# Optimization experiments

Measured on AMD Instinct MI355X. Metric: run time of the kernel, lower is better.

## Reference

```python
import jax, jax.numpy as jnp
import numpy as np

B, L, D, H, DH, M = 2, 2048, 512, 8, 2048, 128  # batch, seq, d_model, heads, d_hidden, max_rel_pos
HD = D // H
EPS = 1e-5


def _ln(x, w, b):
    mu = jnp.mean(x, axis=-1, keepdims=True)
    var = jnp.mean((x - mu) ** 2, axis=-1, keepdims=True)
    return (x - mu) * jax.lax.rsqrt(var + EPS) * w + b


def setup_inputs() -> dict:
    key = jax.random.key(0)
    ks = jax.random.split(key, 8)
    s = 0.02  # init std for weights
    return {
        "x": jax.random.normal(ks[0], (B, L, D), jnp.float32),
        "ln1_w": jnp.ones((D,), jnp.float32),
        "ln1_b": jnp.zeros((D,), jnp.float32),
        "qkv_w": jax.random.normal(ks[1], (D, 3 * D), jnp.float32) * s,
        "qkv_b": jnp.zeros((3 * D,), jnp.float32),
        "out_w": jax.random.normal(ks[2], (D, D), jnp.float32) * s,
        "out_b": jnp.zeros((D,), jnp.float32),
        "rel_bias": jax.random.normal(ks[3], (H, 2 * M - 1), jnp.float32) * s,
        "gamma1": 1e-4 * jnp.ones((D,), jnp.float32),
        "ln2_w": jnp.ones((D,), jnp.float32),
        "ln2_b": jnp.zeros((D,), jnp.float32),
        "ffn_in_w": jax.random.normal(ks[4], (D, 2 * DH), jnp.float32) * s,
        "ffn_in_b": jnp.zeros((2 * DH,), jnp.float32),
        "ffn_out_w": jax.random.normal(ks[5], (DH, D), jnp.float32) * s,
        "ffn_out_b": jnp.zeros((D,), jnp.float32),
        "gamma2": 1e-4 * jnp.ones((D,), jnp.float32),
    }


def _forward(x, ln1_w, ln1_b, qkv_w, qkv_b, out_w, out_b, rel_bias, gamma1,
             ln2_w, ln2_b, ffn_in_w, ffn_in_b, ffn_out_w, ffn_out_b, gamma2):
    b, l, d = x.shape
    # --- PreNorm attention with T5-style relative position bias ---
    h = _ln(x, ln1_w, ln1_b)
    qkv = h @ qkv_w + qkv_b                           # [B, L, 3D]
    q, k, v = jnp.split(qkv, 3, axis=-1)
    q = q.reshape(b, l, H, HD)
    k = k.reshape(b, l, H, HD)
    v = v.reshape(b, l, H, HD)
    scale = 1.0 / jnp.sqrt(jnp.asarray(HD, x.dtype))
    scores = jnp.einsum("bqhd,bkhd->bhqk", q, k) * scale   # [B, H, L, L]
    # relative position bias: clip(i - j) indexed into learned table
    ctx = jnp.arange(l)[:, None] - jnp.arange(l)[None, :]
    ctx = jnp.clip(ctx, -(M - 1), M - 1) + (M - 1)          # [L, L] in [0, 2M-2]
    rel = rel_bias[:, ctx]                                  # [H, L, L]
    scores = scores + rel[None]
    attn = jax.nn.softmax(scores, axis=-1)
    o = jnp.einsum("bhqk,bkhd->bqhd", attn, v).reshape(b, l, d)
    o = o @ out_w + out_b
    x = x + o * gamma1                                      # LayerScale residual
    # --- PreNorm GEGLU FFN ---
    h2 = _ln(x, ln2_w, ln2_b)
    ab = h2 @ ffn_in_w + ffn_in_b                           # [B, L, 2*DH]
    a, bgate = jnp.split(ab, 2, axis=-1)
    f = jax.nn.gelu(bgate, approximate=False) * a
    f = f @ ffn_out_w + ffn_out_b
    x = x + f * gamma2
    return x, attn


def reference(x, ln1_w, ln1_b, qkv_w, qkv_b, out_w, out_b, rel_bias, gamma1,
              ln2_w, ln2_b, ffn_in_w, ffn_in_b, ffn_out_w, ffn_out_b, gamma2):
    return _forward(x, ln1_w, ln1_b, qkv_w, qkv_b, out_w, out_b, rel_bias, gamma1,
                    ln2_w, ln2_b, ffn_in_w, ffn_in_b, ffn_out_w, ffn_out_b, gamma2)
```

## Files before the change

### kernel.cpp

```cpp
#include <hip/hip_runtime.h>
#include <math.h>

typedef __attribute__((ext_vector_type(4))) float f32x4;
typedef __attribute__((ext_vector_type(8))) short bf16x8;
typedef __attribute__((ext_vector_type(4))) short s16x4;

__device__ __forceinline__ unsigned short f2bf(float f) {
  union { float f; unsigned u; } v; v.f = f;
  return (unsigned short)((v.u + 0x7fffu + ((v.u >> 16) & 1u)) >> 16);
}

__global__ void ln_kernel(const float* __restrict__ in, const float* __restrict__ w,
                          const float* __restrict__ b, float* __restrict__ out) {
  __shared__ float sh[4];
  const int t = threadIdx.x;
  const float* p = in + (size_t)blockIdx.x * 512;
  float a0 = p[t], a1 = p[t + 256];
  float s = a0 + a1;
#pragma unroll
  for (int o = 32; o; o >>= 1) s += __shfl_down(s, o);
  if ((t & 63) == 0) sh[t >> 6] = s;
  __syncthreads();
  s = sh[0] + sh[1] + sh[2] + sh[3];
  float mu = s * (1.0f / 512.0f);
  float d0 = a0 - mu, d1 = a1 - mu;
  float q = d0 * d0 + d1 * d1;
  __syncthreads();
#pragma unroll
  for (int o = 32; o; o >>= 1) q += __shfl_down(q, o);
  if ((t & 63) == 0) sh[t >> 6] = q;
  __syncthreads();
  q = sh[0] + sh[1] + sh[2] + sh[3];
  float rstd = rsqrtf(q * (1.0f / 512.0f) + 1e-5f);
  float* po = out + (size_t)blockIdx.x * 512;
  po[t]       = d0 * rstd * w[t] + b[t];
  po[t + 256] = d1 * rstd * w[t + 256] + b[t + 256];
}

__global__ void transpose_w(const float* __restrict__ in, unsigned short* __restrict__ out,
                            int ldi, int ldo, long ibs, long obs) {
  __shared__ float tile[32][33];
  const float* ip = in + (long)blockIdx.z * ibs;
  unsigned short* op = out + (long)blockIdx.z * obs;
  const int tx = threadIdx.x & 31;
  const int ty = threadIdx.x >> 5;
  const int n0 = blockIdx.x * 32, k0 = blockIdx.y * 32;
#pragma unroll
  for (int i = 0; i < 4; ++i)
    tile[ty + i * 8][tx] = ip[(size_t)(k0 + ty + i * 8) * ldi + n0 + tx];
  __syncthreads();
#pragma unroll
  for (int i = 0; i < 4; ++i)
    op[(size_t)(n0 + ty + i * 8) * ldo + k0 + tx] = f2bf(tile[tx][ty + i * 8]);
}

template <int WM, int WN, int TM, int TN, int EPI>
__global__ __launch_bounds__(256) void gemm_kernel(
    const float* __restrict__ A, const unsigned short* __restrict__ Bt,
    float* __restrict__ C, int K, int lda, int ldb, int ldc,
    const float* __restrict__ bias, const float* __restrict__ resid,
    const float* __restrict__ gamma) {
  constexpr int BM = WM * TM * 16;
  constexpr int BN = WN * TN * 16;
  __shared__ short As[BM * 32];
  __shared__ short Bs[BN * 32];

  const int tid = threadIdx.x;
  const int m0 = blockIdx.y * BM, n0 = blockIdx.x * BN;
  const int w = tid >> 6, lane = tid & 63;
  const int wm = w / WN, wn = w % WN;
  const int lrow = lane & 15, lq = lane >> 4;

  f32x4 acc[TM][TN];
#pragma unroll
  for (int i = 0; i < TM; ++i)
#pragma unroll
    for (int j = 0; j < TN; ++j) acc[i][j] = (f32x4){0.f, 0.f, 0.f, 0.f};

  for (int k0 = 0; k0 < K; k0 += 32) {
    __syncthreads();
#pragma unroll
    for (int it = 0; it < (BM * 8) / 256; ++it) {
      int c = it * 256 + tid;
      int row = c >> 3, col = (c & 7) << 2;
      float4 v = *(const float4*)(A + (size_t)(m0 + row) * lda + k0 + col);
      s16x4 r = {(short)f2bf(v.x), (short)f2bf(v.y), (short)f2bf(v.z), (short)f2bf(v.w)};
      *(s16x4*)(As + row * 32 + col) = r;
    }
#pragma unroll
    for (int it = 0; it < (BN * 4) / 256; ++it) {
      int c = it * 256 + tid;
      int row = c >> 2, col = (c & 3) << 3;
      *(bf16x8*)(Bs + row * 32 + col) =
          *(const bf16x8*)(Bt + (size_t)(n0 + row) * ldb + k0 + col);
    }
    __syncthreads();

    bf16x8 af[TM], bf[TN];
#pragma unroll
    for (int mi = 0; mi < TM; ++mi)
      af[mi] = *(const bf16x8*)(As + (wm * TM * 16 + mi * 16 + lrow) * 32 + lq * 8);
#pragma unroll
    for (int nj = 0; nj < TN; ++nj)
      bf[nj] = *(const bf16x8*)(Bs + (wn * TN * 16 + nj * 16 + lrow) * 32 + lq * 8);
#pragma unroll
    for (int mi = 0; mi < TM; ++mi)
#pragma unroll
      for (int nj = 0; nj < TN; ++nj)
        acc[mi][nj] = __builtin_amdgcn_mfma_f32_16x16x32_bf16(af[mi], bf[nj], acc[mi][nj], 0, 0, 0);
  }

#pragma unroll
  for (int mi = 0; mi < TM; ++mi) {
#pragma unroll
    for (int nj = 0; nj < TN; ++nj) {
      int gm0 = m0 + wm * TM * 16 + mi * 16 + lq * 4;
      int gn = n0 + wn * TN * 16 + nj * 16 + lrow;
#pragma unroll
      for (int r = 0; r < 4; ++r) {
        int gm = gm0 + r;
        size_t idx = (size_t)gm * ldc + gn;
        float v = acc[mi][nj][r];
        if constexpr (EPI == 0) {
          C[idx] = v + bias[gn];
        } else {
          C[idx] = resid[idx] + (v + bias[gn]) * gamma[gn];
        }
      }
    }
  }
}

__global__ __launch_bounds__(256) void ffn1_gate_kernel(
    const float* __restrict__ A, const unsigned short* __restrict__ Bt,
    float* __restrict__ F, const float* __restrict__ bias) {
  __shared__ short As[128 * 32];
  __shared__ short Bs[64 * 32];
  __shared__ short Bs2[64 * 32];

  const int tid = threadIdx.x;
  const int n0 = blockIdx.x * 64, m0 = blockIdx.y * 128;
  const int w = tid >> 6, lane = tid & 63;
  const int wm = w >> 1, wn = w & 1;
  const int lrow = lane & 15, lq = lane >> 4;

  f32x4 acca[4][2], accb[4][2];
#pragma unroll
  for (int i = 0; i < 4; ++i)
#pragma unroll
    for (int j = 0; j < 2; ++j) {
      acca[i][j] = (f32x4){0.f, 0.f, 0.f, 0.f};
      accb[i][j] = (f32x4){0.f, 0.f, 0.f, 0.f};
    }

  for (int k0 = 0; k0 < 512; k0 += 32) {
    __syncthreads();
#pragma unroll
    for (int it = 0; it < 4; ++it) {
      int c = it * 256 + tid;
      int row = c >> 3, col = (c & 7) << 2;
      float4 v = *(const float4*)(A + (size_t)(m0 + row) * 512 + k0 + col);
      s16x4 r = {(short)f2bf(v.x), (short)f2bf(v.y), (short)f2bf(v.z), (short)f2bf(v.w)};
      *(s16x4*)(As + row * 32 + col) = r;
    }
    {
      int row = tid >> 2, col = (tid & 3) << 3;
      *(bf16x8*)(Bs + row * 32 + col) =
          *(const bf16x8*)(Bt + (size_t)(n0 + row) * 512 + k0 + col);
      *(bf16x8*)(Bs2 + row * 32 + col) =
          *(const bf16x8*)(Bt + (size_t)(2048 + n0 + row) * 512 + k0 + col);
    }
    __syncthreads();

    bf16x8 af[4], ba[2], bb[2];
#pragma unroll
    for (int mi = 0; mi < 4; ++mi)
      af[mi] = *(const bf16x8*)(As + (wm * 64 + mi * 16 + lrow) * 32 + lq * 8);
#pragma unroll
    for (int nj = 0; nj < 2; ++nj) {
      ba[nj] = *(const bf16x8*)(Bs + (wn * 32 + nj * 16 + lrow) * 32 + lq * 8);
      bb[nj] = *(const bf16x8*)(Bs2 + (wn * 32 + nj * 16 + lrow) * 32 + lq * 8);
    }
#pragma unroll
    for (int mi = 0; mi < 4; ++mi)
#pragma unroll
      for (int nj = 0; nj < 2; ++nj) {
        acca[mi][nj] = __builtin_amdgcn_mfma_f32_16x16x32_bf16(af[mi], ba[nj], acca[mi][nj], 0, 0, 0);
        accb[mi][nj] = __builtin_amdgcn_mfma_f32_16x16x32_bf16(af[mi], bb[nj], accb[mi][nj], 0, 0, 0);
      }
  }

#pragma unroll
  for (int mi = 0; mi < 4; ++mi)
#pragma unroll
    for (int nj = 0; nj < 2; ++nj) {
      int gm0 = m0 + wm * 64 + mi * 16 + lq * 4;
      int gn = n0 + wn * 32 + nj * 16 + lrow;
#pragma unroll
      for (int r = 0; r < 4; ++r) {
        float a = acca[mi][nj][r] + bias[gn];
        float bg = accb[mi][nj][r] + bias[2048 + gn];
        float g = 0.5f * bg * (1.0f + erff(bg * 0.70710678118654752f));
        F[(size_t)(gm0 + r) * 2048 + gn] = g * a;
      }
    }
}

__global__ __launch_bounds__(256) void attn_fused(
    const float* __restrict__ qkv, const unsigned short* __restrict__ vt,
    const float* __restrict__ rel, float* __restrict__ attn, float* __restrict__ o) {
  __shared__ short q_lds[2 * 64 * 32];
  __shared__ short k_lds[2 * 128 * 32];
  __shared__ short p_lds[4 * 64 * 32];
  __shared__ short v_lds[4 * 64 * 32];
  __shared__ float rsum[64];
  __shared__ float rinv[64];

  const int tid = threadIdx.x;
  const int m0 = blockIdx.x * 64;
  const int bh = blockIdx.y;
  const int b = bh >> 3, h = bh & 7;
  const float* qbase = qkv + (size_t)(b * 2048) * 1536 + h * 64;
  const float* kbase = qbase + 512;
  const unsigned short* vbase = vt + (size_t)bh * 64 * 2048;
  float* abase = attn + (size_t)bh * 2048 * 2048;
  const float* relh = rel + h * 255;

  const int w = tid >> 6, lane = tid & 63;
  const int wm = w >> 1, wn = w & 1;
  const int lrow = lane & 15, lq = lane >> 4;

#pragma unroll
  for (int it = 0; it < 4; ++it) {
    int idx = it * 256 + tid;
    int row = idx >> 4, c4 = (idx & 15) << 2;
    float4 v = *(const float4*)(qbase + (size_t)(m0 + row) * 1536 + c4);
    s16x4 r = {(short)f2bf(v.x), (short)f2bf(v.y), (short)f2bf(v.z), (short)f2bf(v.w)};
    *(s16x4*)(q_lds + (c4 >> 5) * 2048 + row * 32 + (c4 & 31)) = r;
  }
  if (tid < 64) rsum[tid] = 0.f;

  float psum[2][4] = {{0.f, 0.f, 0.f, 0.f}, {0.f, 0.f, 0.f, 0.f}};

  for (int t = 0; t < 16; ++t) {
    const int kt0 = t * 128;
    __syncthreads();
#pragma unroll
    for (int it = 0; it < 8; ++it) {
      int idx = it * 256 + tid;
      int row = idx >> 4, c4 = (idx & 15) << 2;
      float4 v = *(const float4*)(kbase + (size_t)(kt0 + row) * 1536 + c4);
      s16x4 r = {(short)f2bf(v.x), (short)f2bf(v.y), (short)f2bf(v.z), (short)f2bf(v.w)};
      *(s16x4*)(k_lds + (c4 >> 5) * 4096 + row * 32 + (c4 & 31)) = r;
    }
    __syncthreads();

    f32x4 acc[2][4];
#pragma unroll
    for (int mi = 0; mi < 2; ++mi)
#pragma unroll
      for (int nj = 0; nj < 4; ++nj) acc[mi][nj] = (f32x4){0.f, 0.f, 0.f, 0.f};
#pragma unroll
    for (int c = 0; c < 2; ++c) {
      bf16x8 af[2], bfv[4];
#pragma unroll
      for (int mi = 0; mi < 2; ++mi)
        af[mi] = *(const bf16x8*)(q_lds + c * 2048 + (wm * 32 + mi * 16 + lrow) * 32 + lq * 8);
#pragma unroll
      for (int nj = 0; nj < 4; ++nj)
        bfv[nj] = *(const bf16x8*)(k_lds + c * 4096 + (wn * 64 + nj * 16 + lrow) * 32 + lq * 8);
#pragma unroll
      for (int mi = 0; mi < 2; ++mi)
#pragma unroll
        for (int nj = 0; nj < 4; ++nj)
          acc[mi][nj] = __builtin_amdgcn_mfma_f32_16x16x32_bf16(af[mi], bfv[nj], acc[mi][nj], 0, 0, 0);
    }
#pragma unroll
    for (int mi = 0; mi < 2; ++mi)
#pragma unroll
      for (int nj = 0; nj < 4; ++nj) {
        int kl = wn * 64 + nj * 16 + lrow;
#pragma unroll
        for (int r = 0; r < 4; ++r) {
          int r_loc = wm * 32 + mi * 16 + lq * 4 + r;
          int d = (m0 + r_loc) - (kt0 + kl);
          d = d < -127 ? -127 : (d > 127 ? 127 : d);
          float s = acc[mi][nj][r] * 0.125f + relh[d + 127];
          psum[mi][r] += __expf(s);
        }
      }
  }
#pragma unroll
  for (int off = 1; off < 16; off <<= 1)
#pragma unroll
    for (int mi = 0; mi < 2; ++mi)
#pragma unroll
      for (int r = 0; r < 4; ++r) psum[mi][r] += __shfl_xor(psum[mi][r], off);
  if (lrow == 0) {
#pragma unroll
    for (int mi = 0; mi < 2; ++mi)
#pragma unroll
      for (int r = 0; r < 4; ++r)
        atomicAdd(&rsum[wm * 32 + mi * 16 + lq * 4 + r], psum[mi][r]);
  }
  __syncthreads();
  if (tid < 64) rinv[tid] = 1.0f / rsum[tid];
  __syncthreads();
  float rv[2][4];
#pragma unroll
  for (int mi = 0; mi < 2; ++mi)
#pragma unroll
    for (int r = 0; r < 4; ++r) rv[mi][r] = rinv[wm * 32 + mi * 16 + lq * 4 + r];

  f32x4 oacc[2][2];
#pragma unroll
  for (int mi = 0; mi < 2; ++mi)
#pragma unroll
    for (int nj = 0; nj < 2; ++nj) oacc[mi][nj] = (f32x4){0.f, 0.f, 0.f, 0.f};

  for (int t = 0; t < 16; ++t) {
    const int kt0 = t * 128;
    __syncthreads();
#pragma unroll
    for (int it = 0; it < 8; ++it) {
      int idx = it * 256 + tid;
      int row = idx >> 4, c4 = (idx & 15) << 2;
      float4 v = *(const float4*)(kbase + (size_t)(kt0 + row) * 1536 + c4);
      s16x4 r = {(short)f2bf(v.x), (short)f2bf(v.y), (short)f2bf(v.z), (short)f2bf(v.w)};
      *(s16x4*)(k_lds + (c4 >> 5) * 4096 + row * 32 + (c4 & 31)) = r;
    }
#pragma unroll
    for (int it = 0; it < 4; ++it) {
      int idx = it * 256 + tid;
      int dd = idx >> 4, c8 = (idx & 15) << 3;
      *(bf16x8*)(v_lds + (c8 >> 5) * 2048 + dd * 32 + (c8 & 31)) =
          *(const bf16x8*)(vbase + (size_t)dd * 2048 + kt0 + c8);
    }
    __syncthreads();

    f32x4 acc[2][4];
#pragma unroll
    for (int mi = 0; mi < 2; ++mi)
#pragma unroll
      for (int nj = 0; nj < 4; ++nj) acc[mi][nj] = (f32x4){0.f, 0.f, 0.f, 0.f};
#pragma unroll
    for (int c = 0; c < 2; ++c) {
      bf16x8 af[2], bfv[4];
#pragma unroll
      for (int mi = 0; mi < 2; ++mi)
        af[mi] = *(const bf16x8*)(q_lds + c * 2048 + (wm * 32 + mi * 16 + lrow) * 32 + lq * 8);
#pragma unroll
      for (int nj = 0; nj < 4; ++nj)
        bfv[nj] = *(const bf16x8*)(k_lds + c * 4096 + (wn * 64 + nj * 16 + lrow) * 32 + lq * 8);
#pragma unroll
      for (int mi = 0; mi < 2; ++mi)
#pragma unroll
        for (int nj = 0; nj < 4; ++nj)
          acc[mi][nj] = __builtin_amdgcn_mfma_f32_16x16x32_bf16(af[mi], bfv[nj], acc[mi][nj], 0, 0, 0);
    }
#pragma unroll
    for (int mi = 0; mi < 2; ++mi)
#pragma unroll
      for (int nj = 0; nj < 4; ++nj) {
        int kl = wn * 64 + nj * 16 + lrow;
#pragma unroll
        for (int r = 0; r < 4; ++r) {
          int r_loc = wm * 32 + mi * 16 + lq * 4 + r;
          int d = (m0 + r_loc) - (kt0 + kl);
          d = d < -127 ? -127 : (d > 127 ? 127 : d);
          float s = acc[mi][nj][r] * 0.125f + relh[d + 127];
          float e = __expf(s) * rv[mi][r];
          __builtin_nontemporal_store(e, abase + (size_t)(m0 + r_loc) * 2048 + kt0 + kl);
          p_lds[(kl >> 5) * 2048 + r_loc * 32 + (kl & 31)] = (short)f2bf(e);
        }
      }
    __syncthreads();

#pragma unroll
    for (int c2 = 0; c2 < 4; ++c2) {
      bf16x8 ap[2], bv[2];
#pragma unroll
      for (int mi = 0; mi < 2; ++mi)
        ap[mi] = *(const bf16x8*)(p_lds + c2 * 2048 + (wm * 32 + mi * 16 + lrow) * 32 + lq * 8);
#pragma unroll
      for (int nj = 0; nj < 2; ++nj)
        bv[nj] = *(const bf16x8*)(v_lds + c2 * 2048 + (wn * 32 + nj * 16 + lrow) * 32 + lq * 8);
#pragma unroll
      for (int mi = 0; mi < 2; ++mi)
#pragma unroll
        for (int nj = 0; nj < 2; ++nj)
          oacc[mi][nj] = __builtin_amdgcn_mfma_f32_16x16x32_bf16(ap[mi], bv[nj], oacc[mi][nj], 0, 0, 0);
    }
  }

#pragma unroll
  for (int mi = 0; mi < 2; ++mi)
#pragma unroll
    for (int nj = 0; nj < 2; ++nj) {
      int dd = wn * 32 + nj * 16 + lrow;
#pragma unroll
      for (int r = 0; r < 4; ++r) {
        int rr = m0 + wm * 32 + mi * 16 + lq * 4 + r;
        o[(size_t)(b * 2048 + rr) * 512 + h * 64 + dd] = oacc[mi][nj][r];
      }
    }
}

extern "C" void kernel_launch(void* const* d_in, const int* in_sizes, int n_in,
                              void* d_out, int out_size, void* d_ws, size_t ws_size,
                              hipStream_t stream) {
  (void)in_sizes; (void)n_in; (void)out_size; (void)ws_size;
  const float* x        = (const float*)d_in[0];
  const float* ln1_w    = (const float*)d_in[1];
  const float* ln1_b    = (const float*)d_in[2];
  const float* qkv_w    = (const float*)d_in[3];
  const float* qkv_b    = (const float*)d_in[4];
  const float* out_w    = (const float*)d_in[5];
  const float* out_b    = (const float*)d_in[6];
  const float* rel_bias = (const float*)d_in[7];
  const float* gamma1   = (const float*)d_in[8];
  const float* ln2_w    = (const float*)d_in[9];
  const float* ln2_b    = (const float*)d_in[10];
  const float* ffn_in_w = (const float*)d_in[11];
  const float* ffn_in_b = (const float*)d_in[12];
  const float* ffn_out_w  = (const float*)d_in[13];
  const float* ffn_out_b  = (const float*)d_in[14];
  const float* gamma2   = (const float*)d_in[15];

  float* x_out = (float*)d_out;
  float* attn  = x_out + (size_t)2 * 2048 * 512;

  float* ws  = (float*)d_ws;
  float* h   = ws;
  float* qkv = h + 2097152;
  float* o   = qkv + 6291456;
  float* x1  = o + 2097152;
  float* f   = x1 + 2097152;
  unsigned short* bt_qkv  = (unsigned short*)(f + 8388608);
  unsigned short* bt_out  = bt_qkv + 786432;
  unsigned short* bt_ffn1 = bt_out + 262144;
  unsigned short* bt_ffn2 = bt_ffn1 + 2097152;
  unsigned short* vt      = bt_ffn2 + 1048576;

  transpose_w<<<dim3(48, 16, 1), 256, 0, stream>>>(qkv_w,     bt_qkv,  1536, 512,  0, 0);
  transpose_w<<<dim3(16, 16, 1), 256, 0, stream>>>(out_w,     bt_out,  512,  512,  0, 0);
  transpose_w<<<dim3(128, 16, 1), 256, 0, stream>>>(ffn_in_w, bt_ffn1, 4096, 512,  0, 0);
  transpose_w<<<dim3(16, 64, 1), 256, 0, stream>>>(ffn_out_w, bt_ffn2, 512,  2048, 0, 0);

  ln_kernel<<<4096, 256, 0, stream>>>(x, ln1_w, ln1_b, h);

  gemm_kernel<2, 2, 4, 4, 0><<<dim3(12, 32, 1), 256, 0, stream>>>(
      h, bt_qkv, qkv, 512, 512, 512, 1536, qkv_b, nullptr, nullptr);

  transpose_w<<<dim3(2, 64, 8), 256, 0, stream>>>(
      qkv + 1024, vt, 1536, 2048, 64, (long)64 * 2048);
  transpose_w<<<dim3(2, 64, 8), 256, 0, stream>>>(
      qkv + (size_t)2048 * 1536 + 1024, vt + (size_t)8 * 64 * 2048, 1536, 2048, 64,
      (long)64 * 2048);

  attn_fused<<<dim3(32, 16, 1), 256, 0, stream>>>(qkv, vt, rel_bias, attn, o);

  gemm_kernel<2, 2, 4, 4, 3><<<dim3(4, 32, 1), 256, 0, stream>>>(
      o, bt_out, x1, 512, 512, 512, 512, out_b, x, gamma1);

  ln_kernel<<<4096, 256, 0, stream>>>(x1, ln2_w, ln2_b, h);

  ffn1_gate_kernel<<<dim3(32, 32, 1), 256, 0, stream>>>(h, bt_ffn1, f, ffn_in_b);

  gemm_kernel<2, 2, 4, 4, 3><<<dim3(4, 32, 1), 256, 0, stream>>>(
      f, bt_ffn2, x_out, 2048, 2048, 2048, 512, ffn_out_b, x1, gamma2);
}
```

Baseline: 641.6 us.

## Rework attention kernel to read bf16 operands directly and shrink tiles

The QKV GEMM now also writes a bf16 copy of its output, so the attention kernel loads Q/K fragments straight from global memory into registers and no longer converts and stages them in LDS. The attention tile shrinks to 32 query rows, with swizzled block ordering and a per-wave P buffer that uses an XOR swizzle. The relative-bias exponentials are precomputed once per block, and key tiles far from the diagonal take a constant-bias fast path. The GEMM tile sizes are also halved to launch more blocks. The exchange is more redundant global K/V reads per block and extra bf16 writes, in return for fewer block barriers and less LDS traffic.

```diff
diff --git a/kernel.cpp b/kernel.cpp
--- a/kernel.cpp
+++ b/kernel.cpp
@@ -57,7 +57,8 @@
 template <int WM, int WN, int TM, int TN, int EPI>
 __global__ __launch_bounds__(256) void gemm_kernel(
     const float* __restrict__ A, const unsigned short* __restrict__ Bt,
-    float* __restrict__ C, int K, int lda, int ldb, int ldc,
+    float* __restrict__ C, unsigned short* __restrict__ Cbf,
+    int K, int lda, int ldb, int ldc,
     const float* __restrict__ bias, const float* __restrict__ resid,
     const float* __restrict__ gamma) {
   constexpr int BM = WM * TM * 16;
@@ -123,6 +124,10 @@
         float v = acc[mi][nj][r];
         if constexpr (EPI == 0) {
           C[idx] = v + bias[gn];
+        } else if constexpr (EPI == 4) {
+          float u = v + bias[gn];
+          C[idx] = u;
+          Cbf[idx] = f2bf(u);
         } else {
           C[idx] = resid[idx] + (v + bias[gn]) * gamma[gn];
         }
@@ -206,204 +211,193 @@
     }
 }
 
-__global__ __launch_bounds__(256) void attn_fused(
-    const float* __restrict__ qkv, const unsigned short* __restrict__ vt,
+__global__ __launch_bounds__(256, 4) void attn_fused(
+    const unsigned short* __restrict__ qkvbf, const unsigned short* __restrict__ vt,
     const float* __restrict__ rel, float* __restrict__ attn, float* __restrict__ o) {
-  __shared__ short q_lds[2 * 64 * 32];
-  __shared__ short k_lds[2 * 128 * 32];
-  __shared__ short p_lds[4 * 64 * 32];
-  __shared__ short v_lds[4 * 64 * 32];
-  __shared__ float rsum[64];
-  __shared__ float rinv[64];
+  __shared__ __align__(16) short p_lds[4 * 16 * 64];
+  __shared__ float erel[256];
+  __shared__ float rsum[32];
+  __shared__ float rinv[32];
 
   const int tid = threadIdx.x;
-  const int m0 = blockIdx.x * 64;
-  const int bh = blockIdx.y;
+  const int flat = blockIdx.y * 64 + blockIdx.x;
+  const int swz = (flat & 7) * 128 + (flat >> 3);
+  const int bh = swz >> 6;
+  const int m0 = (swz & 63) * 32;
   const int b = bh >> 3, h = bh & 7;
-  const float* qbase = qkv + (size_t)(b * 2048) * 1536 + h * 64;
-  const float* kbase = qbase + 512;
-  const unsigned short* vbase = vt + (size_t)bh * 64 * 2048;
-  float* abase = attn + (size_t)bh * 2048 * 2048;
-  const float* relh = rel + h * 255;
 
   const int w = tid >> 6, lane = tid & 63;
   const int wm = w >> 1, wn = w & 1;
   const int lrow = lane & 15, lq = lane >> 4;
 
-#pragma unroll
-  for (int it = 0; it < 4; ++it) {
-    int idx = it * 256 + tid;
-    int row = idx >> 4, c4 = (idx & 15) << 2;
-    float4 v = *(const float4*)(qbase + (size_t)(m0 + row) * 1536 + c4);
-    s16x4 r = {(short)f2bf(v.x), (short)f2bf(v.y), (short)f2bf(v.z), (short)f2bf(v.w)};
-    *(s16x4*)(q_lds + (c4 >> 5) * 2048 + row * 32 + (c4 & 31)) = r;
-  }
-  if (tid < 64) rsum[tid] = 0.f;
-
-  float psum[2][4] = {{0.f, 0.f, 0.f, 0.f}, {0.f, 0.f, 0.f, 0.f}};
-
+  const unsigned short* qb = qkvbf + (size_t)(b * 2048) * 1536 + h * 64;
+  const unsigned short* kb = qb + 512;
+  const unsigned short* vb = vt + (size_t)bh * 64 * 2048;
+  float* ab = attn + (size_t)bh * 2048 * 2048;
+  const float* relh = rel + h * 255;
+
+  if (tid < 32) rsum[tid] = 0.f;
+  if (tid < 255) erel[tid] = __expf(relh[tid]);
+
+  bf16x8 qf[2];
+#pragma unroll
+  for (int c = 0; c < 2; ++c)
+    qf[c] = *(const bf16x8*)(qb + (size_t)(m0 + wm * 16 + lrow) * 1536 + c * 32 + lq * 8);
+
+  const unsigned short* krow = kb + (size_t)(wn * 64 + lrow) * 1536 + lq * 8;
+  const unsigned short* vrow = vb + (size_t)lrow * 2048 + wn * 64 + lq * 8;
+
+  const float C = 0.125f * 1.44269504088896f;
+
+  __syncthreads();
+
+  float psum[4] = {0.f, 0.f, 0.f, 0.f};
+  const int dbase = (m0 + wm * 16 + lq * 4) - (wn * 64 + lrow);
   for (int t = 0; t < 16; ++t) {
     const int kt0 = t * 128;
-    __syncthreads();
-#pragma unroll
-    for (int it = 0; it < 8; ++it) {
-      int idx = it * 256 + tid;
-      int row = idx >> 4, c4 = (idx & 15) << 2;
-      float4 v = *(const float4*)(kbase + (size_t)(kt0 + row) * 1536 + c4);
-      s16x4 r = {(short)f2bf(v.x), (short)f2bf(v.y), (short)f2bf(v.z), (short)f2bf(v.w)};
-      *(s16x4*)(k_lds + (c4 >> 5) * 4096 + row * 32 + (c4 & 31)) = r;
-    }
-    __syncthreads();
-
-    f32x4 acc[2][4];
-#pragma unroll
-    for (int mi = 0; mi < 2; ++mi)
-#pragma unroll
-      for (int nj = 0; nj < 4; ++nj) acc[mi][nj] = (f32x4){0.f, 0.f, 0.f, 0.f};
+    f32x4 acc[4];
+#pragma unroll
+    for (int nj = 0; nj < 4; ++nj) acc[nj] = (f32x4){0.f, 0.f, 0.f, 0.f};
 #pragma unroll
     for (int c = 0; c < 2; ++c) {
-      bf16x8 af[2], bfv[4];
-#pragma unroll
-      for (int mi = 0; mi < 2; ++mi)
-        af[mi] = *(const bf16x8*)(q_lds + c * 2048 + (wm * 32 + mi * 16 + lrow) * 32 + lq * 8);
-#pragma unroll
-      for (int nj = 0; nj < 4; ++nj)
-        bfv[nj] = *(const bf16x8*)(k_lds + c * 4096 + (wn * 64 + nj * 16 + lrow) * 32 + lq * 8);
-#pragma unroll
-      for (int mi = 0; mi < 2; ++mi)
-#pragma unroll
-        for (int nj = 0; nj < 4; ++nj)
-          acc[mi][nj] = __builtin_amdgcn_mfma_f32_16x16x32_bf16(af[mi], bfv[nj], acc[mi][nj], 0, 0, 0);
-    }
-#pragma unroll
-    for (int mi = 0; mi < 2; ++mi)
+      bf16x8 kf[4];
+#pragma unroll
+      for (int nj = 0; nj < 4; ++nj)
+        kf[nj] = *(const bf16x8*)(krow + (size_t)(kt0 + nj * 16) * 1536 + c * 32);
+#pragma unroll
+      for (int nj = 0; nj < 4; ++nj)
+        acc[nj] = __builtin_amdgcn_mfma_f32_16x16x32_bf16(qf[c], kf[nj], acc[nj], 0, 0, 0);
+    }
+    const int Dt = m0 - kt0;
+    if (Dt >= 256 || Dt <= -160) {
+      float ec = erel[Dt >= 256 ? 254 : 0];
+#pragma unroll
+      for (int r = 0; r < 4; ++r) {
+        float s = 0.f;
+#pragma unroll
+        for (int nj = 0; nj < 4; ++nj) s += exp2f(acc[nj][r] * C);
+        psum[r] += ec * s;
+      }
+    } else {
 #pragma unroll
       for (int nj = 0; nj < 4; ++nj) {
-        int kl = wn * 64 + nj * 16 + lrow;
+        int d0 = dbase - kt0 - nj * 16;
 #pragma unroll
         for (int r = 0; r < 4; ++r) {
-          int r_loc = wm * 32 + mi * 16 + lq * 4 + r;
-          int d = (m0 + r_loc) - (kt0 + kl);
+          int d = d0 + r;
           d = d < -127 ? -127 : (d > 127 ? 127 : d);
-          float s = acc[mi][nj][r] * 0.125f + relh[d + 127];
-          psum[mi][r] += __expf(s);
+          psum[r] += exp2f(acc[nj][r] * C) * erel[d + 127];
         }
       }
+    }
   }
 #pragma unroll
   for (int off = 1; off < 16; off <<= 1)
 #pragma unroll
-    for (int mi = 0; mi < 2; ++mi)
-#pragma unroll
-      for (int r = 0; r < 4; ++r) psum[mi][r] += __shfl_xor(psum[mi][r], off);
+    for (int r = 0; r < 4; ++r) psum[r] += __shfl_xor(psum[r], off);
   if (lrow == 0) {
 #pragma unroll
-    for (int mi = 0; mi < 2; ++mi)
-#pragma unroll
-      for (int r = 0; r < 4; ++r)
-        atomicAdd(&rsum[wm * 32 + mi * 16 + lq * 4 + r], psum[mi][r]);
-  }
-  __syncthreads();
-  if (tid < 64) rinv[tid] = 1.0f / rsum[tid];
-  __syncthreads();
-  float rv[2][4];
-#pragma unroll
-  for (int mi = 0; mi < 2; ++mi)
-#pragma unroll
-    for (int r = 0; r < 4; ++r) rv[mi][r] = rinv[wm * 32 + mi * 16 + lq * 4 + r];
-
-  f32x4 oacc[2][2];
-#pragma unroll
-  for (int mi = 0; mi < 2; ++mi)
-#pragma unroll
-    for (int nj = 0; nj < 2; ++nj) oacc[mi][nj] = (f32x4){0.f, 0.f, 0.f, 0.f};
+    for (int r = 0; r < 4; ++r) atomicAdd(&rsum[wm * 16 + lq * 4 + r], psum[r]);
+  }
+  __syncthreads();
+  if (tid < 32) rinv[tid] = 1.0f / rsum[tid];
+  __syncthreads();
+  float rv[4];
+#pragma unroll
+  for (int r = 0; r < 4; ++r) rv[r] = rinv[wm * 16 + lq * 4 + r];
+
+  f32x4 oacc[4];
+#pragma unroll
+  for (int nj = 0; nj < 4; ++nj) oacc[nj] = (f32x4){0.f, 0.f, 0.f, 0.f};
+  short* pw = p_lds + w * (16 * 64);
 
   for (int t = 0; t < 16; ++t) {
     const int kt0 = t * 128;
-    __syncthreads();
-#pragma unroll
-    for (int it = 0; it < 8; ++it) {
-      int idx = it * 256 + tid;
-      int row = idx >> 4, c4 = (idx & 15) << 2;
-      float4 v = *(const float4*)(kbase + (size_t)(kt0 + row) * 1536 + c4);
-      s16x4 r = {(short)f2bf(v.x), (short)f2bf(v.y), (short)f2bf(v.z), (short)f2bf(v.w)};
-      *(s16x4*)(k_lds + (c4 >> 5) * 4096 + row * 32 + (c4 & 31)) = r;
-    }
-#pragma unroll
-    for (int it = 0; it < 4; ++it) {
-      int idx = it * 256 + tid;
-      int dd = idx >> 4, c8 = (idx & 15) << 3;
-      *(bf16x8*)(v_lds + (c8 >> 5) * 2048 + dd * 32 + (c8 & 31)) =
-          *(const bf16x8*)(vbase + (size_t)dd * 2048 + kt0 + c8);
-    }
-    __syncthreads();
-
-    f32x4 acc[2][4];
-#pragma unroll
-    for (int mi = 0; mi < 2; ++mi)
-#pragma unroll
-      for (int nj = 0; nj < 4; ++nj) acc[mi][nj] = (f32x4){0.f, 0.f, 0.f, 0.f};
+    f32x4 acc[4];
+#pragma unroll
+    for (int nj = 0; nj < 4; ++nj) acc[nj] = (f32x4){0.f, 0.f, 0.f, 0.f};
 #pragma unroll
     for (int c = 0; c < 2; ++c) {
-      bf16x8 af[2], bfv[4];
-#pragma unroll
-      for (int mi = 0; mi < 2; ++mi)
-        af[mi] = *(const bf16x8*)(q_lds + c * 2048 + (wm * 32 + mi * 16 + lrow) * 32 + lq * 8);
-#pragma unroll
-      for (int nj = 0; nj < 4; ++nj)
-        bfv[nj] = *(const bf16x8*)(k_lds + c * 4096 + (wn * 64 + nj * 16 + lrow) * 32 + lq * 8);
-#pragma unroll
-      for (int mi = 0; mi < 2; ++mi)
-#pragma unroll
-        for (int nj = 0; nj < 4; ++nj)
-          acc[mi][nj] = __builtin_amdgcn_mfma_f32_16x16x32_bf16(af[mi], bfv[nj], acc[mi][nj], 0, 0, 0);
-    }
-#pragma unroll
-    for (int mi = 0; mi < 2; ++mi)
-#pragma unroll
-      for (int nj = 0; nj < 4; ++nj) {
-        int kl = wn * 64 + nj * 16 + lrow;
-#pragma unroll
-        for (int r = 0; r < 4; ++r) {
-          int r_loc = wm * 32 + mi * 16 + lq * 4 + r;
-          int d = (m0 + r_loc) - (kt0 + kl);
+      bf16x8 kf[4];
+#pragma unroll
+      for (int nj = 0; nj < 4; ++nj)
+        kf[nj] = *(const bf16x8*)(krow + (size_t)(kt0 + nj * 16) * 1536 + c * 32);
+#pragma unroll
+      for (int nj = 0; nj < 4; ++nj)
+        acc[nj] = __builtin_amdgcn_mfma_f32_16x16x32_bf16(qf[c], kf[nj], acc[nj], 0, 0, 0);
+    }
+
+    const int Dt = m0 - kt0;
+    if (Dt >= 256 || Dt <= -160) {
+      float ec = erel[Dt >= 256 ? 254 : 0];
+#pragma unroll
+      for (int r = 0; r < 4; ++r) {
+        float fr = ec * rv[r];
+        int prow = lq * 4 + r;
+        size_t arow = (size_t)(m0 + wm * 16 + prow) * 2048 + kt0 + wn * 64 + lrow;
+#pragma unroll
+        for (int nj = 0; nj < 4; ++nj) {
+          float e = exp2f(acc[nj][r] * C) * fr;
+          __builtin_nontemporal_store(e, ab + arow + nj * 16);
+          int byte = prow * 128 + ((((nj * 16 + lrow) << 1)) ^ ((prow & 7) << 4));
+          *(short*)((char*)pw + byte) = (short)f2bf(e);
+        }
+      }
+    } else {
+#pragma unroll
+      for (int r = 0; r < 4; ++r) {
+        int prow = lq * 4 + r;
+        size_t arow = (size_t)(m0 + wm * 16 + prow) * 2048 + kt0 + wn * 64 + lrow;
+        int d0 = dbase - kt0 + r;
+#pragma unroll
+        for (int nj = 0; nj < 4; ++nj) {
+          int d = d0 - nj * 16;
           d = d < -127 ? -127 : (d > 127 ? 127 : d);
-          float s = acc[mi][nj][r] * 0.125f + relh[d + 127];
-          float e = __expf(s) * rv[mi][r];
-          __builtin_nontemporal_store(e, abase + (size_t)(m0 + r_loc) * 2048 + kt0 + kl);
-          p_lds[(kl >> 5) * 2048 + r_loc * 32 + (kl & 31)] = (short)f2bf(e);
+          float e = exp2f(acc[nj][r] * C) * erel[d + 127] * rv[r];
+          __builtin_nontemporal_store(e, ab + arow + nj * 16);
+          int byte = prow * 128 + ((((nj * 16 + lrow) << 1)) ^ ((prow & 7) << 4));
+          *(short*)((char*)pw + byte) = (short)f2bf(e);
         }
       }
-    __syncthreads();
-
-#pragma unroll
-    for (int c2 = 0; c2 < 4; ++c2) {
-      bf16x8 ap[2], bv[2];
-#pragma unroll
-      for (int mi = 0; mi < 2; ++mi)
-        ap[mi] = *(const bf16x8*)(p_lds + c2 * 2048 + (wm * 32 + mi * 16 + lrow) * 32 + lq * 8);
-#pragma unroll
-      for (int nj = 0; nj < 2; ++nj)
-        bv[nj] = *(const bf16x8*)(v_lds + c2 * 2048 + (wn * 32 + nj * 16 + lrow) * 32 + lq * 8);
-#pragma unroll
-      for (int mi = 0; mi < 2; ++mi)
-#pragma unroll
-        for (int nj = 0; nj < 2; ++nj)
-          oacc[mi][nj] = __builtin_amdgcn_mfma_f32_16x16x32_bf16(ap[mi], bv[nj], oacc[mi][nj], 0, 0, 0);
-    }
-  }
-
-#pragma unroll
-  for (int mi = 0; mi < 2; ++mi)
-#pragma unroll
-    for (int nj = 0; nj < 2; ++nj) {
-      int dd = wn * 32 + nj * 16 + lrow;
-#pragma unroll
-      for (int r = 0; r < 4; ++r) {
-        int rr = m0 + wm * 32 + mi * 16 + lq * 4 + r;
-        o[(size_t)(b * 2048 + rr) * 512 + h * 64 + dd] = oacc[mi][nj][r];
-      }
-    }
+    }
+
+#pragma unroll
+    for (int c2 = 0; c2 < 2; ++c2) {
+      bf16x8 ap;
+      {
+        int byte = lrow * 128 + ((c2 * 64 + lq * 16) ^ ((lrow & 7) << 4));
+        ap = *(const bf16x8*)((char*)pw + byte);
+      }
+      bf16x8 bv[4];
+#pragma unroll
+      for (int nj = 0; nj < 4; ++nj)
+        bv[nj] = *(const bf16x8*)(vrow + (size_t)(nj * 16) * 2048 + kt0 + c2 * 32);
+#pragma unroll
+      for (int nj = 0; nj < 4; ++nj)
+        oacc[nj] = __builtin_amdgcn_mfma_f32_16x16x32_bf16(ap, bv[nj], oacc[nj], 0, 0, 0);
+    }
+  }
+
+  __syncthreads();
+  float* osc = (float*)p_lds;
+  if (wn == 0) {
+#pragma unroll
+    for (int nj = 0; nj < 4; ++nj)
+#pragma unroll
+      for (int r = 0; r < 4; ++r)
+        osc[(wm * 16 + lq * 4 + r) * 64 + nj * 16 + lrow] = oacc[nj][r];
+  }
+  __syncthreads();
+  if (wn == 1) {
+#pragma unroll
+    for (int nj = 0; nj < 4; ++nj)
+#pragma unroll
+      for (int r = 0; r < 4; ++r) {
+        int rr = m0 + wm * 16 + lq * 4 + r;
+        float v = oacc[nj][r] + osc[(wm * 16 + lq * 4 + r) * 64 + nj * 16 + lrow];
+        o[(size_t)(b * 2048 + rr) * 512 + h * 64 + nj * 16 + lrow] = v;
+      }
+  }
 }
 
 extern "C" void kernel_launch(void* const* d_in, const int* in_sizes, int n_in,
@@ -441,6 +435,7 @@
   unsigned short* bt_ffn1 = bt_out + 262144;
   unsigned short* bt_ffn2 = bt_ffn1 + 2097152;
   unsigned short* vt      = bt_ffn2 + 1048576;
+  unsigned short* qkvbf   = (unsigned short*)f;
 
   transpose_w<<<dim3(48, 16, 1), 256, 0, stream>>>(qkv_w,     bt_qkv,  1536, 512,  0, 0);
   transpose_w<<<dim3(16, 16, 1), 256, 0, stream>>>(out_w,     bt_out,  512,  512,  0, 0);
@@ -449,8 +444,8 @@
 
   ln_kernel<<<4096, 256, 0, stream>>>(x, ln1_w, ln1_b, h);
 
-  gemm_kernel<2, 2, 4, 4, 0><<<dim3(12, 32, 1), 256, 0, stream>>>(
-      h, bt_qkv, qkv, 512, 512, 512, 1536, qkv_b, nullptr, nullptr);
+  gemm_kernel<2, 2, 2, 4, 4><<<dim3(12, 64, 1), 256, 0, stream>>>(
+      h, bt_qkv, qkv, qkvbf, 512, 512, 512, 1536, qkv_b, nullptr, nullptr);
 
   transpose_w<<<dim3(2, 64, 8), 256, 0, stream>>>(
       qkv + 1024, vt, 1536, 2048, 64, (long)64 * 2048);
@@ -458,15 +453,15 @@
       qkv + (size_t)2048 * 1536 + 1024, vt + (size_t)8 * 64 * 2048, 1536, 2048, 64,
       (long)64 * 2048);
 
-  attn_fused<<<dim3(32, 16, 1), 256, 0, stream>>>(qkv, vt, rel_bias, attn, o);
-
-  gemm_kernel<2, 2, 4, 4, 3><<<dim3(4, 32, 1), 256, 0, stream>>>(
-      o, bt_out, x1, 512, 512, 512, 512, out_b, x, gamma1);
+  attn_fused<<<dim3(64, 16, 1), 256, 0, stream>>>(qkvbf, vt, rel_bias, attn, o);
+
+  gemm_kernel<2, 2, 2, 4, 3><<<dim3(4, 64, 1), 256, 0, stream>>>(
+      o, bt_out, x1, nullptr, 512, 512, 512, 512, out_b, x, gamma1);
 
   ln_kernel<<<4096, 256, 0, stream>>>(x1, ln2_w, ln2_b, h);
 
   ffn1_gate_kernel<<<dim3(32, 32, 1), 256, 0, stream>>>(h, bt_ffn1, f, ffn_in_b);
 
-  gemm_kernel<2, 2, 4, 4, 3><<<dim3(4, 32, 1), 256, 0, stream>>>(
-      f, bt_ffn2, x_out, 2048, 2048, 2048, 512, ffn_out_b, x1, gamma2);
-}
+  gemm_kernel<2, 2, 2, 4, 3><<<dim3(4, 64, 1), 256, 0, stream>>>(
+      f, bt_ffn2, x_out, nullptr, 2048, 2048, 2048, 512, ffn_out_b, x1, gamma2);
+}
```

Result: faster. 601.2 us (-6.3%).
